# Optimization experiments

Measured on AMD Instinct MI355X. Metric: run time of the kernel, lower is better.

## Reference

```python
import jax, jax.numpy as jnp
import numpy as np
from jax import lax

COMMITMENT_COST = 0.25

def setup_inputs() -> dict:
    key = jax.random.key(0)
    k1, k2, k3, k4 = jax.random.split(key, 4)
    B, C, H, W, K = 32, 128, 32, 32, 8192
    return {
        "x": jax.random.normal(k1, (B, C, H, W), dtype=jnp.float32),
        "W_lin": jax.random.normal(k2, (C, C), dtype=jnp.float32) * (1.0 / np.sqrt(C)),
        "b_lin": jax.random.normal(k3, (C,), dtype=jnp.float32) * 0.01,
        "emb": jax.random.normal(k4, (K, C), dtype=jnp.float32),
    }

def reference(x, W_lin, b_lin, emb):
    B, C, H, W = x.shape
    K = emb.shape[0]
    # BCHW -> BHWC, then linear projection
    inp = jnp.transpose(x, (0, 2, 3, 1))          # [B,H,W,C]
    inp = inp @ W_lin.T + b_lin                   # nn.Linear
    flat = inp.reshape(-1, C)                     # [N,C], N=B*H*W
    # squared L2 distances to codebook: ||z||^2 + ||e||^2 - 2 z.e
    d = (jnp.sum(flat**2, axis=1, keepdims=True)
         + jnp.sum(emb**2, axis=1)
         - 2.0 * flat @ emb.T)                    # [N,K]
    idx = jnp.argmin(d, axis=1)                   # [N]
    quantized = emb[idx].reshape(inp.shape)       # gather == onehot @ emb
    e_latent = jnp.mean((lax.stop_gradient(quantized) - inp) ** 2)
    q_latent = jnp.mean((quantized - lax.stop_gradient(inp)) ** 2)
    loss = q_latent + COMMITMENT_COST * e_latent
    # straight-through estimator
    quantized_st = inp + lax.stop_gradient(quantized - inp)
    # perplexity from code usage histogram (== mean of one-hot encodings)
    counts = jnp.zeros((K,), dtype=flat.dtype).at[idx].add(1.0)
    avg_probs = counts / flat.shape[0]
    perplexity = jnp.exp(-jnp.sum(avg_probs * jnp.log(avg_probs + 1e-10)))
    out = jnp.transpose(quantized_st, (0, 3, 1, 2))  # back to BCHW
    return (loss, out, perplexity, idx[:, None])
```

## Files before the change

kernel.cpp:

```cpp
#include <hip/hip_runtime.h>
#include <hip/hip_bf16.h>
#include <float.h>

#define NPIX   32768
#define CDIM   128
#define KCB    8192
#define EPS_STOP 0.30f
#define TAUF   0.012f
#define RCAP   8192
#define RCAPA  2048

typedef _Float16 f16x8 __attribute__((ext_vector_type(8)));
typedef float    f32x16 __attribute__((ext_vector_type(16)));

#define WS_EMBFH   0
#define WS_E2      2359296
#define WS_ZWS     2392064
#define WS_CAND    19169280
#define WS_IDX     20217856
#define WS_RLISTA  20348928
#define WS_RLISTB  20381696
#define WS_SCAND   20512768
#define WS_SCANI   21037056
#define WS_COUNTS  21299200
#define WS_LOSS    21331968
#define WS_RCNTA   21331972
#define WS_RCNTB   21331976
#define WS_ZERO_OFF 21299200
#define WS_ZERO_LEN 32780

#define OUT_OFF_OUT  1
#define OUT_OFF_PERP 4194305
#define OUT_OFF_IDX  4194306

__device__ __forceinline__ float min3f(float a, float b, float c) {
    return fminf(fminf(a, b), c);
}

__device__ __forceinline__ void ins6(float f, float v[6]) {
    float a = fmaxf(v[0], f); v[0] = fminf(v[0], f);
    float b = fmaxf(v[1], a); v[1] = fminf(v[1], a);
    a = fmaxf(v[2], b); v[2] = fminf(v[2], b);
    b = fmaxf(v[3], a); v[3] = fminf(v[3], a);
    a = fmaxf(v[4], b); v[4] = fminf(v[4], b);
    v[5] = fminf(v[5], a);
}

__device__ __forceinline__ float packmin(float m, uint32_t id) {
    return __uint_as_float((__float_as_uint(m) & 0xFFFFFE00u) | id);
}

__global__ __launch_bounds__(256) void k_e2(const float* __restrict__ emb, float* __restrict__ e2) {
    int t = threadIdx.x;
    int wv = t >> 6, l = t & 63;
    int k = blockIdx.x * 4 + wv;
    const float2 v = *(const float2*)&emb[(size_t)k * 128 + l * 2];
    float s = v.x * v.x + v.y * v.y;
    #pragma unroll
    for (int o = 32; o; o >>= 1) s += __shfl_down(s, o, 64);
    if (l == 0) e2[k] = s;
}

__global__ __launch_bounds__(256) void k_prep(const float* __restrict__ emb, const float* __restrict__ e2,
                                              _Float16* __restrict__ embFh) {
    int tid = blockIdx.x * 256 + threadIdx.x;
    int m = tid / 18, r = tid % 18;
    int s = r >> 1, h = r & 1;
    f16x8 hv;
    #pragma unroll
    for (int j = 0; j < 8; ++j) hv[j] = (_Float16)0.0f;
    if (s < 8) {
        int c0 = s * 16 + h * 8;
        const float4 a = *(const float4*)&emb[(size_t)m * 128 + c0];
        const float4 b = *(const float4*)&emb[(size_t)m * 128 + c0 + 4];
        float vals[8] = {a.x, a.y, a.z, a.w, b.x, b.y, b.z, b.w};
        #pragma unroll
        for (int j = 0; j < 8; ++j) hv[j] = (_Float16)(-2.0f * vals[j]);
    } else if (h == 0) {
        float v = e2[m] + 512.0f;
        _Float16 eh = (_Float16)v;
        hv[0] = eh;
        hv[1] = (_Float16)(v - (float)eh);
    }
    size_t base = (((size_t)(m >> 5) * 9 + s) * 64 + (m & 31) + h * 32) * 8;
    *(f16x8*)&embFh[base] = hv;
}

__global__ __launch_bounds__(256, 2) void k_main(
    const float* __restrict__ x, const float* __restrict__ Wl, const float* __restrict__ bl,
    const _Float16* __restrict__ embFh,
    float* __restrict__ zws, float4* __restrict__ cand)
{
    __shared__ __align__(16) float As[64 * 132];
    __shared__ __align__(16) float Xs[64 * 66];
    __shared__ float z2p[256];

    const int t  = threadIdx.x;
    const int n0 = blockIdx.x * 64;
    const int b  = n0 >> 10;
    const int hw0 = n0 & 1023;

    {
        const int p = t & 63, ig = t >> 6;
        float accz[32];
        const float4* bl4 = (const float4*)(bl + ig * 32);
        #pragma unroll
        for (int q = 0; q < 8; ++q) {
            float4 v = bl4[q];
            accz[4*q+0] = v.x; accz[4*q+1] = v.y; accz[4*q+2] = v.z; accz[4*q+3] = v.w;
        }
        for (int hf = 0; hf < 2; ++hf) {
            __syncthreads();
            for (int r = 0; r < 16; ++r) {
                int lin = r * 256 + t;
                int cc = lin >> 6, pp = lin & 63;
                Xs[cc * 66 + pp] = x[(size_t)(b * 128 + hf * 64 + cc) * 1024 + hw0 + pp];
            }
            __syncthreads();
            for (int cc4 = 0; cc4 < 16; ++cc4) {
                float xv0 = Xs[(cc4*4+0) * 66 + p];
                float xv1 = Xs[(cc4*4+1) * 66 + p];
                float xv2 = Xs[(cc4*4+2) * 66 + p];
                float xv3 = Xs[(cc4*4+3) * 66 + p];
                #pragma unroll
                for (int ii = 0; ii < 32; ++ii) {
                    const float4 w4 = *(const float4*)&Wl[(size_t)(ig*32+ii) * 128 + hf*64 + cc4*4];
                    float a = accz[ii];
                    a = fmaf(w4.x, xv0, a);
                    a = fmaf(w4.y, xv1, a);
                    a = fmaf(w4.z, xv2, a);
                    a = fmaf(w4.w, xv3, a);
                    accz[ii] = a;
                }
            }
        }
        float ssq = 0.f;
        float4* ao = (float4*)&As[p * 132 + ig * 32];
        float4* zo = (float4*)(zws + (size_t)(n0 + p) * 128 + ig * 32);
        #pragma unroll
        for (int q = 0; q < 8; ++q) {
            float4 v = make_float4(accz[4*q+0], accz[4*q+1], accz[4*q+2], accz[4*q+3]);
            ao[q] = v;
            zo[q] = v;
            ssq = fmaf(v.x, v.x, fmaf(v.y, v.y, fmaf(v.z, v.z, fmaf(v.w, v.w, ssq))));
        }
        z2p[p * 4 + ig] = ssq;
    }
    __syncthreads();

    const int l = t & 63, w = t >> 6;
    const int half = l >> 5, pcol = l & 31;
    f16x8 B0[9], B1[9];
    #pragma unroll
    for (int nt = 0; nt < 2; ++nt) {
        int p = nt * 32 + pcol;
        #pragma unroll
        for (int s = 0; s < 8; ++s) {
            const float* zp = &As[p * 132 + s * 16 + half * 8];
            float4 v0 = *(const float4*)zp;
            float4 v1 = *(const float4*)(zp + 4);
            float vals[8] = {v0.x, v0.y, v0.z, v0.w, v1.x, v1.y, v1.z, v1.w};
            f16x8 hh;
            #pragma unroll
            for (int j2 = 0; j2 < 8; ++j2) hh[j2] = (_Float16)vals[j2];
            if (nt == 0) B0[s] = hh; else B1[s] = hh;
        }
    }
    {
        f16x8 b8;
        #pragma unroll
        for (int j2 = 0; j2 < 8; ++j2) b8[j2] = (_Float16)0.0f;
        if (half == 0) { b8[0] = (_Float16)1.0f; b8[1] = (_Float16)1.0f; }
        B0[8] = b8; B1[8] = b8;
    }

    auto tree16 = [](const f32x16& v) -> float {
        float a = min3f(v[0], v[1], v[2]);
        float bb = min3f(v[3], v[4], v[5]);
        float c = min3f(v[6], v[7], v[8]);
        float d = min3f(v[9], v[10], v[11]);
        float e = min3f(v[12], v[13], v[14]);
        float f = min3f(a, bb, c);
        float g = min3f(d, e, v[15]);
        return fminf(f, g);
    };

    float gv[6] = {3e38f, 3e38f, 3e38f, 3e38f, 3e38f, 3e38f};
    float hv[6] = {3e38f, 3e38f, 3e38f, 3e38f, 3e38f, 3e38f};
    const f16x8* Ahp = (const f16x8*)embFh;
    f16x8 aE[9], aO[9];
    {
        const f16x8* P = Ahp + (size_t)w * 576 + l;
        #pragma unroll
        for (int s = 0; s < 9; ++s) aE[s] = P[s * 64];
    }
    {
        const f16x8* P = Ahp + (size_t)(w + 4) * 576 + l;
        #pragma unroll
        for (int s = 0; s < 9; ++s) aO[s] = P[s * 64];
    }

    f32x16 e0, e1, o0, o1;
    uint32_t idv = (uint32_t)((w << 1) | half);

    e0 = {}; e1 = {};
    #pragma unroll
    for (int s = 0; s < 9; ++s) {
        e0 = __builtin_amdgcn_mfma_f32_32x32x16_f16(aE[s], B0[s], e0, 0, 0, 0);
        e1 = __builtin_amdgcn_mfma_f32_32x32x16_f16(aE[s], B1[s], e1, 0, 0, 0);
    }

    for (int it = 0; it < 31; ++it) {
        const int g = w + it * 8;
        {
            const f16x8* P = Ahp + (size_t)(g + 8) * 576 + l;
            #pragma unroll
            for (int s = 0; s < 9; ++s) aE[s] = P[s * 64];
        }
        o0 = {}; o1 = {};
        #pragma unroll
        for (int s = 0; s < 9; ++s) {
            o0 = __builtin_amdgcn_mfma_f32_32x32x16_f16(aO[s], B0[s], o0, 0, 0, 0);
            o1 = __builtin_amdgcn_mfma_f32_32x32x16_f16(aO[s], B1[s], o1, 0, 0, 0);
        }
        {
            float m0 = tree16(e0), m1 = tree16(e1);
            ins6(packmin(m0, idv), gv);
            ins6(packmin(m1, idv), hv);
        }
        {
            const f16x8* P = Ahp + (size_t)(g + 12) * 576 + l;
            #pragma unroll
            for (int s = 0; s < 9; ++s) aO[s] = P[s * 64];
        }
        e0 = {}; e1 = {};
        #pragma unroll
        for (int s = 0; s < 9; ++s) {
            e0 = __builtin_amdgcn_mfma_f32_32x32x16_f16(aE[s], B0[s], e0, 0, 0, 0);
            e1 = __builtin_amdgcn_mfma_f32_32x32x16_f16(aE[s], B1[s], e1, 0, 0, 0);
        }
        {
            float m0 = tree16(o0), m1 = tree16(o1);
            ins6(packmin(m0, idv + 8u), gv);
            ins6(packmin(m1, idv + 8u), hv);
        }
        idv += 16u;
    }
    o0 = {}; o1 = {};
    #pragma unroll
    for (int s = 0; s < 9; ++s) {
        o0 = __builtin_amdgcn_mfma_f32_32x32x16_f16(aO[s], B0[s], o0, 0, 0, 0);
        o1 = __builtin_amdgcn_mfma_f32_32x32x16_f16(aO[s], B1[s], o1, 0, 0, 0);
    }
    {
        float m0 = tree16(e0), m1 = tree16(e1);
        ins6(packmin(m0, idv), gv);
        ins6(packmin(m1, idv), hv);
    }
    {
        float m0 = tree16(o0), m1 = tree16(o1);
        ins6(packmin(m0, idv + 8u), gv);
        ins6(packmin(m1, idv + 8u), hv);
    }

    __syncthreads();
    float* Ms = Xs;
    const int slot = (w << 1) | half;
    #pragma unroll
    for (int q = 0; q < 6; ++q) {
        Ms[(pcol * 8 + slot) * 6 + q] = gv[q];
        Ms[((32 + pcol) * 8 + slot) * 6 + q] = hv[q];
    }
    __syncthreads();
    if (t < 64) {
        float v6[6] = {3e38f, 3e38f, 3e38f, 3e38f, 3e38f, 3e38f};
        #pragma unroll
        for (int s = 0; s < 48; ++s) ins6(Ms[t * 48 + s], v6);
        float z2 = z2p[t*4+0] + z2p[t*4+1] + z2p[t*4+2] + z2p[t*4+3];
        cand[(size_t)(n0 + t) * 2 + 0] = make_float4(v6[0], v6[1], v6[2], v6[3]);
        cand[(size_t)(n0 + t) * 2 + 1] = make_float4(v6[4], v6[5], z2, 0.f);
    }
}

__global__ __launch_bounds__(256) void k_rec(
    const float* __restrict__ zws, const float* __restrict__ emb,
    const float4* __restrict__ cand, int* __restrict__ idxws,
    float* __restrict__ out_idxf, float* __restrict__ losssum,
    int* __restrict__ rlistA, int* __restrict__ rcntA,
    int* __restrict__ rlistB, int* __restrict__ rcntB)
{
    __shared__ float lred[16];
    const int t = threadIdx.x;
    const int pl = t >> 4, j = t & 15;
    const int n = blockIdx.x * 16 + pl;

    const float4 za = *(const float4*)&zws[(size_t)n * 128 + j * 8];
    const float4 zb = *(const float4*)&zws[(size_t)n * 128 + j * 8 + 4];
    const float4 c0 = cand[(size_t)n * 2 + 0];
    const float4 c1 = cand[(size_t)n * 2 + 1];
    const float pv[6] = {c0.x, c0.y, c0.z, c0.w, c1.x, c1.y};
    const float pbase = c1.z - 512.0f;

    float d1 = 3e38f, d2 = 3e38f; int i1 = 0x7fffffff, i2 = 0x7fffffff;
    bool safe = false;
    float lastgmin = 0.f;
    for (int q = 0; q < 6; ++q) {
        uint32_t bits = __float_as_uint(pv[q]);
        float gmin = __uint_as_float(bits & 0xFFFFFE00u);
        lastgmin = gmin;
        if (gmin >= d1 - pbase + EPS_STOP) { safe = true; break; }
        const int mbase = (int)((bits >> 1) & 255u) * 32 + (int)((bits & 1u) << 2);
        #pragma unroll
        for (int c = 0; c < 16; ++c) {
            int m = mbase + (c & 3) + 8 * (c >> 2);
            const float4 ea = *(const float4*)&emb[(size_t)m * 128 + j * 8];
            const float4 eb = *(const float4*)&emb[(size_t)m * 128 + j * 8 + 4];
            float da0 = za.x - ea.x, da1 = za.y - ea.y, da2 = za.z - ea.z, da3 = za.w - ea.w;
            float db0 = zb.x - eb.x, db1 = zb.y - eb.y, db2 = zb.z - eb.z, db3 = zb.w - eb.w;
            float s = da0*da0; s = fmaf(da1, da1, s); s = fmaf(da2, da2, s); s = fmaf(da3, da3, s);
            s = fmaf(db0, db0, s); s = fmaf(db1, db1, s); s = fmaf(db2, db2, s); s = fmaf(db3, db3, s);
            s += __shfl_xor(s, 1, 16);
            s += __shfl_xor(s, 2, 16);
            s += __shfl_xor(s, 4, 16);
            s += __shfl_xor(s, 8, 16);
            if (s < d1 || (s == d1 && m < i1)) { d2 = d1; i2 = i1; d1 = s; i1 = m; }
            else if (s < d2) { d2 = s; i2 = m; }
        }
    }
    if (!safe && lastgmin >= d1 - pbase + EPS_STOP) safe = true;

    if (j == 0) {
        idxws[n] = i1;
        out_idxf[n] = (float)i1;
        if (!safe) {
            int s = atomicAdd(rcntA, 1);
            if (s < RCAPA) rlistA[s] = n;
        } else if ((d2 - d1) < TAUF) {
            int s = atomicAdd(rcntB, 1);
            if (s < RCAP) { int4 v4 = make_int4(n, i1, i2, 0); ((int4*)rlistB)[s] = v4; }
        }
        lred[pl] = d1;
    }
    __syncthreads();
    if (t == 0) {
        float ls = 0.f;
        #pragma unroll
        for (int q = 0; q < 16; ++q) ls += lred[q];
        atomicAdd(losssum, ls);
    }
}

__global__ __launch_bounds__(256) void k_scanp(
    const float* __restrict__ zws, const float* __restrict__ emb,
    const int* __restrict__ rcntA, const int* __restrict__ rlistA,
    double* __restrict__ scand, int* __restrict__ scani)
{
    int cnt = *rcntA; if (cnt > RCAPA) cnt = RCAPA;
    const int t = threadIdx.x;
    const int chunk = blockIdx.x & 31;
    const int gi = t >> 4, j = t & 15;
    __shared__ double sd[16];
    __shared__ int si[16];
    for (int e = blockIdx.x >> 5; e < cnt; e += 64) {
        const int n = rlistA[e];
        const float4 za = *(const float4*)&zws[(size_t)n * 128 + j * 8];
        const float4 zb = *(const float4*)&zws[(size_t)n * 128 + j * 8 + 4];
        double best = 1e300; int bi = 0x7fffffff;
        const int kbase = chunk * 256 + gi * 16;
        for (int c = 0; c < 16; ++c) {
            const int m = kbase + c;
            const float4 ea = *(const float4*)&emb[(size_t)m * 128 + j * 8];
            const float4 eb = *(const float4*)&emb[(size_t)m * 128 + j * 8 + 4];
            double s = 0.0, d;
            d = (double)za.x - (double)ea.x; s += d * d;
            d = (double)za.y - (double)ea.y; s += d * d;
            d = (double)za.z - (double)ea.z; s += d * d;
            d = (double)za.w - (double)ea.w; s += d * d;
            d = (double)zb.x - (double)eb.x; s += d * d;
            d = (double)zb.y - (double)eb.y; s += d * d;
            d = (double)zb.z - (double)eb.z; s += d * d;
            d = (double)zb.w - (double)eb.w; s += d * d;
            s += __shfl_xor(s, 1, 16);
            s += __shfl_xor(s, 2, 16);
            s += __shfl_xor(s, 4, 16);
            s += __shfl_xor(s, 8, 16);
            if (s < best) { best = s; bi = m; }
        }
        __syncthreads();
        if (j == 0) { sd[gi] = best; si[gi] = bi; }
        __syncthreads();
        if (t == 0) {
            double b = sd[0]; int ib = si[0];
            #pragma unroll
            for (int q = 1; q < 16; ++q)
                if (sd[q] < b || (sd[q] == b && si[q] < ib)) { b = sd[q]; ib = si[q]; }
            scand[e * 32 + chunk] = b;
            scani[e * 32 + chunk] = ib;
        }
    }
}

__global__ __launch_bounds__(64) void k_mergeA(
    const int* __restrict__ rcntA, const int* __restrict__ rlistA,
    const double* __restrict__ scand, const int* __restrict__ scani,
    int* __restrict__ idxws, float* __restrict__ out_idxf)
{
    int cnt = *rcntA; if (cnt > RCAPA) cnt = RCAPA;
    const int t = threadIdx.x;
    for (int e = blockIdx.x; e < cnt; e += gridDim.x) {
        double b = 1e300; int ib = 0x7fffffff;
        if (t < 32) { b = scand[e * 32 + t]; ib = scani[e * 32 + t]; }
        #pragma unroll
        for (int o = 16; o; o >>= 1) {
            double ob = __shfl_down(b, o, 64);
            int oi = __shfl_down(ib, o, 64);
            if (ob < b || (ob == b && oi < ib)) { b = ob; ib = oi; }
        }
        if (t == 0) { int n = rlistA[e]; idxws[n] = ib; out_idxf[n] = (float)ib; }
    }
}

__global__ __launch_bounds__(128) void k_pairB(
    const float* __restrict__ x, const float* __restrict__ Wl, const float* __restrict__ bl,
    const float* __restrict__ emb, const int* __restrict__ rcntB, const int* __restrict__ rlistB,
    int* __restrict__ idxws, float* __restrict__ out_idxf)
{
    __shared__ double xs[128];
    __shared__ double red[128];
    int cnt = *rcntB; if (cnt > RCAP) cnt = RCAP;
    const int t = threadIdx.x;
    for (int e = blockIdx.x; e < cnt; e += gridDim.x) {
        const int4 v = ((const int4*)rlistB)[e];
        const int n = v.x, c1 = v.y, c2 = v.z;
        const int b = n >> 10, hw = n & 1023;
        __syncthreads();
        xs[t] = (double)x[(size_t)(b * 128 + t) * 1024 + hw];
        __syncthreads();
        double z = (double)bl[t];
        for (int c = 0; c < 128; ++c) z = fma((double)Wl[(size_t)t * 128 + c], xs[c], z);
        double d1v, d2v;
        double da = z - (double)emb[(size_t)c1 * 128 + t];
        red[t] = da * da; __syncthreads();
        for (int o = 64; o; o >>= 1) { if (t < o) red[t] += red[t + o]; __syncthreads(); }
        d1v = red[0]; __syncthreads();
        double db = z - (double)emb[(size_t)c2 * 128 + t];
        red[t] = db * db; __syncthreads();
        for (int o = 64; o; o >>= 1) { if (t < o) red[t] += red[t + o]; __syncthreads(); }
        d2v = red[0];
        if (t == 0) {
            int win = (d2v < d1v || (d2v == d1v && c2 < c1)) ? c2 : c1;
            idxws[n] = win;
            out_idxf[n] = (float)win;
        }
        __syncthreads();
    }
}

__global__ __launch_bounds__(256) void k_out(
    const float* __restrict__ emb, const int* __restrict__ idxws,
    float* __restrict__ outp , float* __restrict__ counts)
{
    const int t = threadIdx.x;
    const int b = blockIdx.x >> 2, h0 = (blockIdx.x & 3) << 3;
    const int n = b * 1024 + h0 * 32 + t;
    const int id = idxws[n];
    atomicAdd(&counts[id], 1.0f);
    const float4* ep = (const float4*)&emb[(size_t)id * 128];
    float* ob = outp + (size_t)b * 131072 + h0 * 32 + t;
    #pragma unroll 4
    for (int c4 = 0; c4 < 32; ++c4) {
        float4 v = ep[c4];
        ob[(c4 * 4 + 0) * 1024] = v.x;
        ob[(c4 * 4 + 1) * 1024] = v.y;
        ob[(c4 * 4 + 2) * 1024] = v.z;
        ob[(c4 * 4 + 3) * 1024] = v.w;
    }
}

__global__ __launch_bounds__(256) void k_final(
    const float* __restrict__ counts, const float* __restrict__ losssum, float* __restrict__ d_out)
{
    const int t = threadIdx.x;
    float ent = 0.f;
    for (int k = t; k < KCB; k += 256) {
        float p = counts[k] * (1.0f / 32768.0f);
        ent -= p * logf(p + 1e-10f);
    }
    #pragma unroll
    for (int o = 32; o; o >>= 1) ent += __shfl_down(ent, o, 64);
    __shared__ float wred[4];
    if ((t & 63) == 0) wred[t >> 6] = ent;
    __syncthreads();
    if (t == 0) {
        float e = wred[0] + wred[1] + wred[2] + wred[3];
        d_out[0] = 1.25f * (*losssum) * (1.0f / 4194304.0f);
        d_out[OUT_OFF_PERP] = expf(e);
    }
}

extern "C" void kernel_launch(void* const* d_in, const int* in_sizes, int n_in,
                              void* d_out, int out_size, void* d_ws, size_t ws_size,
                              hipStream_t stream) {
    (void)in_sizes; (void)n_in; (void)out_size; (void)ws_size;
    const float* x   = (const float*)d_in[0];
    const float* Wl  = (const float*)d_in[1];
    const float* bl  = (const float*)d_in[2];
    const float* emb = (const float*)d_in[3];
    float* out = (float*)d_out;
    char*  ws  = (char*)d_ws;

    _Float16* embFh = (_Float16*)(ws + WS_EMBFH);
    float* e2      = (float*)(ws + WS_E2);
    float* zws     = (float*)(ws + WS_ZWS);
    float4* cand   = (float4*)(ws + WS_CAND);
    int*   idxws   = (int*)  (ws + WS_IDX);
    int*   rlistA  = (int*)  (ws + WS_RLISTA);
    int*   rlistB  = (int*)  (ws + WS_RLISTB);
    double* scand  = (double*)(ws + WS_SCAND);
    int*   scani   = (int*)  (ws + WS_SCANI);
    float* counts  = (float*)(ws + WS_COUNTS);
    float* losssum = (float*)(ws + WS_LOSS);
    int*   rcntA   = (int*)  (ws + WS_RCNTA);
    int*   rcntB   = (int*)  (ws + WS_RCNTB);

    hipMemsetAsync(ws + WS_ZERO_OFF, 0, WS_ZERO_LEN, stream);

    k_e2<<<KCB / 4, 256, 0, stream>>>(emb, e2);
    k_prep<<<576, 256, 0, stream>>>(emb, e2, embFh);
    k_main<<<NPIX / 64, 256, 0, stream>>>(x, Wl, bl, embFh, zws, cand);
    k_rec<<<NPIX / 16, 256, 0, stream>>>(zws, emb, cand, idxws, out + OUT_OFF_IDX,
                                         losssum, rlistA, rcntA, rlistB, rcntB);
    k_scanp<<<2048, 256, 0, stream>>>(zws, emb, rcntA, rlistA, scand, scani);
    k_mergeA<<<32, 64, 0, stream>>>(rcntA, rlistA, scand, scani, idxws, out + OUT_OFF_IDX);
    k_pairB<<<256, 128, 0, stream>>>(x, Wl, bl, emb, rcntB, rlistB, idxws, out + OUT_OFF_IDX);
    k_out<<<128, 256, 0, stream>>>(emb, idxws, out + OUT_OFF_OUT, counts);
    k_final<<<1, 256, 0, stream>>>(counts, losssum, out);
}
```

Measured before the change: 288.6 us.

## Raise MFMA wave priority, fuse mergeA and pairB kernels, use nontemporal output stores

Wraps each MFMA burst in the main distance kernel with s_setprio(1)/s_setprio(0) so waves issuing matrix ops get scheduler priority over waves doing loads and reductions. Merges the small k_mergeA and k_pairB kernels into one k_fix launch: the first 32 blocks do the merge and the remaining 256 do the pair recheck, which removes one launch and its serialization gap. Output stores in k_out become nontemporal to avoid polluting cache. The priority hints may not help if the MFMA pipe is already saturated, and the fused kernel runs 128-thread blocks where half the threads sit idle in the merge path.

```diff
diff --git a/kernel.cpp b/kernel.cpp
--- a/kernel.cpp
+++ b/kernel.cpp
@@ -204,11 +204,13 @@
     uint32_t idv = (uint32_t)((w << 1) | half);
 
     e0 = {}; e1 = {};
+    __builtin_amdgcn_s_setprio(1);
     #pragma unroll
     for (int s = 0; s < 9; ++s) {
         e0 = __builtin_amdgcn_mfma_f32_32x32x16_f16(aE[s], B0[s], e0, 0, 0, 0);
         e1 = __builtin_amdgcn_mfma_f32_32x32x16_f16(aE[s], B1[s], e1, 0, 0, 0);
     }
+    __builtin_amdgcn_s_setprio(0);
 
     for (int it = 0; it < 31; ++it) {
         const int g = w + it * 8;
@@ -218,11 +220,13 @@
             for (int s = 0; s < 9; ++s) aE[s] = P[s * 64];
         }
         o0 = {}; o1 = {};
+        __builtin_amdgcn_s_setprio(1);
         #pragma unroll
         for (int s = 0; s < 9; ++s) {
             o0 = __builtin_amdgcn_mfma_f32_32x32x16_f16(aO[s], B0[s], o0, 0, 0, 0);
             o1 = __builtin_amdgcn_mfma_f32_32x32x16_f16(aO[s], B1[s], o1, 0, 0, 0);
         }
+        __builtin_amdgcn_s_setprio(0);
         {
             float m0 = tree16(e0), m1 = tree16(e1);
             ins6(packmin(m0, idv), gv);
@@ -234,11 +238,13 @@
             for (int s = 0; s < 9; ++s) aO[s] = P[s * 64];
         }
         e0 = {}; e1 = {};
+        __builtin_amdgcn_s_setprio(1);
         #pragma unroll
         for (int s = 0; s < 9; ++s) {
             e0 = __builtin_amdgcn_mfma_f32_32x32x16_f16(aE[s], B0[s], e0, 0, 0, 0);
             e1 = __builtin_amdgcn_mfma_f32_32x32x16_f16(aE[s], B1[s], e1, 0, 0, 0);
         }
+        __builtin_amdgcn_s_setprio(0);
         {
             float m0 = tree16(o0), m1 = tree16(o1);
             ins6(packmin(m0, idv + 8u), gv);
@@ -247,11 +253,13 @@
         idv += 16u;
     }
     o0 = {}; o1 = {};
+    __builtin_amdgcn_s_setprio(1);
     #pragma unroll
     for (int s = 0; s < 9; ++s) {
         o0 = __builtin_amdgcn_mfma_f32_32x32x16_f16(aO[s], B0[s], o0, 0, 0, 0);
         o1 = __builtin_amdgcn_mfma_f32_32x32x16_f16(aO[s], B1[s], o1, 0, 0, 0);
     }
+    __builtin_amdgcn_s_setprio(0);
     {
         float m0 = tree16(e0), m1 = tree16(e1);
         ins6(packmin(m0, idv), gv);
@@ -400,36 +408,36 @@
     }
 }
 
-__global__ __launch_bounds__(64) void k_mergeA(
+__global__ __launch_bounds__(128) void k_fix(
+    const float* __restrict__ x, const float* __restrict__ Wl, const float* __restrict__ bl,
+    const float* __restrict__ emb,
     const int* __restrict__ rcntA, const int* __restrict__ rlistA,
     const double* __restrict__ scand, const int* __restrict__ scani,
+    const int* __restrict__ rcntB, const int* __restrict__ rlistB,
     int* __restrict__ idxws, float* __restrict__ out_idxf)
 {
-    int cnt = *rcntA; if (cnt > RCAPA) cnt = RCAPA;
     const int t = threadIdx.x;
-    for (int e = blockIdx.x; e < cnt; e += gridDim.x) {
-        double b = 1e300; int ib = 0x7fffffff;
-        if (t < 32) { b = scand[e * 32 + t]; ib = scani[e * 32 + t]; }
-        #pragma unroll
-        for (int o = 16; o; o >>= 1) {
-            double ob = __shfl_down(b, o, 64);
-            int oi = __shfl_down(ib, o, 64);
-            if (ob < b || (ob == b && oi < ib)) { b = ob; ib = oi; }
-        }
-        if (t == 0) { int n = rlistA[e]; idxws[n] = ib; out_idxf[n] = (float)ib; }
-    }
-}
-
-__global__ __launch_bounds__(128) void k_pairB(
-    const float* __restrict__ x, const float* __restrict__ Wl, const float* __restrict__ bl,
-    const float* __restrict__ emb, const int* __restrict__ rcntB, const int* __restrict__ rlistB,
-    int* __restrict__ idxws, float* __restrict__ out_idxf)
-{
+    if (blockIdx.x < 32) {
+        if (t < 64) {
+            int cnt = *rcntA; if (cnt > RCAPA) cnt = RCAPA;
+            for (int e = blockIdx.x; e < cnt; e += 32) {
+                double b = 1e300; int ib = 0x7fffffff;
+                if (t < 32) { b = scand[e * 32 + t]; ib = scani[e * 32 + t]; }
+                #pragma unroll
+                for (int o = 16; o; o >>= 1) {
+                    double ob = __shfl_down(b, o, 64);
+                    int oi = __shfl_down(ib, o, 64);
+                    if (ob < b || (ob == b && oi < ib)) { b = ob; ib = oi; }
+                }
+                if (t == 0) { int n = rlistA[e]; idxws[n] = ib; out_idxf[n] = (float)ib; }
+            }
+        }
+        return;
+    }
     __shared__ double xs[128];
     __shared__ double red[128];
     int cnt = *rcntB; if (cnt > RCAP) cnt = RCAP;
-    const int t = threadIdx.x;
-    for (int e = blockIdx.x; e < cnt; e += gridDim.x) {
+    for (int e = (int)blockIdx.x - 32; e < cnt; e += 256) {
         const int4 v = ((const int4*)rlistB)[e];
         const int n = v.x, c1 = v.y, c2 = v.z;
         const int b = n >> 10, hw = n & 1023;
@@ -470,10 +478,10 @@
     #pragma unroll 4
     for (int c4 = 0; c4 < 32; ++c4) {
         float4 v = ep[c4];
-        ob[(c4 * 4 + 0) * 1024] = v.x;
-        ob[(c4 * 4 + 1) * 1024] = v.y;
-        ob[(c4 * 4 + 2) * 1024] = v.z;
-        ob[(c4 * 4 + 3) * 1024] = v.w;
+        __builtin_nontemporal_store(v.x, &ob[(c4 * 4 + 0) * 1024]);
+        __builtin_nontemporal_store(v.y, &ob[(c4 * 4 + 1) * 1024]);
+        __builtin_nontemporal_store(v.z, &ob[(c4 * 4 + 2) * 1024]);
+        __builtin_nontemporal_store(v.w, &ob[(c4 * 4 + 3) * 1024]);
     }
 }
 
@@ -531,8 +539,8 @@
     k_rec<<<NPIX / 16, 256, 0, stream>>>(zws, emb, cand, idxws, out + OUT_OFF_IDX,
                                          losssum, rlistA, rcntA, rlistB, rcntB);
     k_scanp<<<2048, 256, 0, stream>>>(zws, emb, rcntA, rlistA, scand, scani);
-    k_mergeA<<<32, 64, 0, stream>>>(rcntA, rlistA, scand, scani, idxws, out + OUT_OFF_IDX);
-    k_pairB<<<256, 128, 0, stream>>>(x, Wl, bl, emb, rcntB, rlistB, idxws, out + OUT_OFF_IDX);
+    k_fix<<<288, 128, 0, stream>>>(x, Wl, bl, emb, rcntA, rlistA, scand, scani,
+                                   rcntB, rlistB, idxws, out + OUT_OFF_IDX);
     k_out<<<128, 256, 0, stream>>>(emb, idxws, out + OUT_OFF_OUT, counts);
     k_final<<<1, 256, 0, stream>>>(counts, losssum, out);
 }
```

New measurement: 296.9 us. +2.9%, slower.
